# Kernel tuning notes

Measured on AMD Instinct MI355X. Metric: run time of the kernel, lower is better.

Reference implementation:

```python
import jax, jax.numpy as jnp
import numpy as np

B, N, D, F = 32, 4096, 256, 256

def setup_inputs() -> dict:
    key = jax.random.key(0)
    k1, k2, k3, k4 = jax.random.split(key, 4)
    raw_input = jax.random.normal(k1, (B, N, D), dtype=jnp.float32)
    input_plus_attention = jax.random.normal(k2, (B, F), dtype=jnp.float32)
    W = jax.random.normal(k3, (F, N), dtype=jnp.float32) * 0.02
    b = jnp.zeros((N,), dtype=jnp.float32)
    # keras 'uniform' initializer: U(-0.05, 0.05)
    threshold = jax.random.uniform(k4, (1,), minval=-0.05, maxval=0.05, dtype=jnp.float32)
    return {"raw_input": raw_input, "input_plus_attention": input_plus_attention,
            "W": W, "b": b, "threshold": threshold}

def reference(raw_input, input_plus_attention, W, b, threshold):
    # Dense(units, relu): [B,F] @ [F,N] -> [B,N]
    x = jax.nn.relu(input_plus_attention @ W + b)
    # BinaryLayer: 1.0 where x > threshold else 0.0 -> row selection mask [B,N]
    mask = x > threshold[0]
    # TF boolean_mask + reshape(B,-1,D) performs per-batch stream compaction of
    # selected rows. JAX needs static shapes, so compact selected rows to the
    # front (stable order preserved) and zero-pad the tail to length N.
    order = jnp.argsort(jnp.where(mask, 0, 1).astype(jnp.int32), axis=1)  # stable: selected first
    gathered = jnp.take_along_axis(raw_input, order[:, :, None], axis=1)  # [B,N,D]
    counts = jnp.sum(mask, axis=1, keepdims=True)                          # [B,1]
    keep = jnp.arange(N)[None, :] < counts                                 # [B,N]
    out = jnp.where(keep[:, :, None], gathered, jnp.zeros((), raw_input.dtype))
    return out
```

## Files before the change

### kernel.cpp

```cpp
#include <hip/hip_runtime.h>
#include <hip/hip_bf16.h>
#include <stdint.h>


#define BB 32
#define NN 4096
#define DD 256
#define FF 256
#define COLS 16
#define CH (NN / COLS)
#define ASTRIDE (FF + 4)
#define ROWS_PER_BLK 8

typedef float f4 __attribute__((ext_vector_type(4)));

__global__ __launch_bounds__(256) void mask_kernel(
    const float* __restrict__ A,
    const float* __restrict__ W,
    const float* __restrict__ bias,
    const float* __restrict__ thr_p,
    uint16_t* __restrict__ bits)
{
    __shared__ float a_sh[BB * ASTRIDE];
    __shared__ float wT[COLS * ASTRIDE];

    const int t     = threadIdx.x;
    const int chunk = blockIdx.x;
    const int n0    = chunk * COLS;

    for (int i = t; i < BB * FF; i += 256) {
        int b = i >> 8, f = i & 255;
        a_sh[b * ASTRIDE + f] = A[i];
    }
    for (int i = t; i < FF * COLS; i += 256) {
        int f = i >> 4, c = i & 15;
        wT[c * ASTRIDE + f] = W[(size_t)f * NN + n0 + c];
    }
    __syncthreads();

    const float thr = thr_p[0];
    const int c  = t & 15;
    const int b1 = t >> 4;
    const int b2 = b1 + 16;

    const f4* a1p = reinterpret_cast<const f4*>(a_sh + b1 * ASTRIDE);
    const f4* a2p = reinterpret_cast<const f4*>(a_sh + b2 * ASTRIDE);
    const f4* wp  = reinterpret_cast<const f4*>(wT   + c  * ASTRIDE);

    double s0 = 0.0, s1 = 0.0, s2 = 0.0, s3 = 0.0;
    #pragma unroll 8
    for (int fs = 0; fs < FF / 4; ++fs) {
        f4 w4 = wp[fs];
        f4 a1 = a1p[fs];
        f4 a2 = a2p[fs];
        s0 = fma((double)a1.x, (double)w4.x, s0);
        s0 = fma((double)a1.y, (double)w4.y, s0);
        s1 = fma((double)a1.z, (double)w4.z, s1);
        s1 = fma((double)a1.w, (double)w4.w, s1);
        s2 = fma((double)a2.x, (double)w4.x, s2);
        s2 = fma((double)a2.y, (double)w4.y, s2);
        s3 = fma((double)a2.z, (double)w4.z, s3);
        s3 = fma((double)a2.w, (double)w4.w, s3);
    }
    const float bi = bias[n0 + c];
    const float v1 = (float)(s0 + s1) + bi;
    const float v2 = (float)(s2 + s3) + bi;
    const int m1 = (fmaxf(v1, 0.f) > thr) ? 1 : 0;
    const int m2 = (fmaxf(v2, 0.f) > thr) ? 1 : 0;

    unsigned long long bal1 = __ballot(m1);
    unsigned long long bal2 = __ballot(m2);
    if (c == 0) {
        const int g = (t & 63) >> 4;
        bits[b1 * CH + chunk] = (uint16_t)((bal1 >> (16 * g)) & 0xFFFF);
        bits[b2 * CH + chunk] = (uint16_t)((bal2 >> (16 * g)) & 0xFFFF);
    }
}

__global__ __launch_bounds__(256) void gather_kernel(
    const float* __restrict__ raw,
    const uint16_t* __restrict__ bits,
    float* __restrict__ out)
{
    const int b   = blockIdx.y;
    const int t   = threadIdx.x;
    const int j0b = blockIdx.x * ROWS_PER_BLK;

    __shared__ int wsum[4];
    __shared__ int cnt_sh;
    __shared__ int order_sh[ROWS_PER_BLK];

    unsigned m = bits[b * CH + t];
    const int s = __popc(m);

    const int lane = t & 63;
    const int wid  = t >> 6;
    int incl = s;
    #pragma unroll
    for (int d = 1; d < 64; d <<= 1) {
        int x = __shfl_up(incl, d, 64);
        if (lane >= d) incl += x;
    }
    if (lane == 63) wsum[wid] = incl;
    __syncthreads();
    if (t == 0) {
        int run = 0;
        #pragma unroll
        for (int i = 0; i < 4; ++i) { int x = wsum[i]; wsum[i] = run; run += x; }
        cnt_sh = run;
    }
    __syncthreads();

    int base = wsum[wid] + (incl - s);
    if (base < j0b + ROWS_PER_BLK && base + s > j0b) {
        const int n0 = t * COLS;
        while (m) {
            const int pos = __ffs(m) - 1;
            const unsigned rel = (unsigned)(base - j0b);
            if (rel < ROWS_PER_BLK) order_sh[rel] = n0 + pos;
            ++base;
            if (base >= j0b + ROWS_PER_BLK) break;
            m &= m - 1;
        }
    }
    __syncthreads();

    const int cnt = cnt_sh;
    const f4* rawp = reinterpret_cast<const f4*>(raw);
    f4* outp = reinterpret_cast<f4*>(out);
    const int j0 = j0b + wid * 2;

    f4 r0 = {0.f, 0.f, 0.f, 0.f};
    f4 r1 = {0.f, 0.f, 0.f, 0.f};
    if (j0 < cnt) {
        const int src = order_sh[j0 - j0b];
        r0 = __builtin_nontemporal_load(rawp + ((size_t)b * NN + src) * (DD / 4) + lane);
    }
    if (j0 + 1 < cnt) {
        const int src = order_sh[j0 + 1 - j0b];
        r1 = __builtin_nontemporal_load(rawp + ((size_t)b * NN + src) * (DD / 4) + lane);
    }
    __builtin_nontemporal_store(r0, outp + ((size_t)b * NN + j0)     * (DD / 4) + lane);
    __builtin_nontemporal_store(r1, outp + ((size_t)b * NN + j0 + 1) * (DD / 4) + lane);
}

extern "C" void kernel_launch(void* const* d_in, const int* in_sizes, int n_in,
                              void* d_out, int out_size, void* d_ws, size_t ws_size,
                              hipStream_t stream) {
    const float* raw  = (const float*)d_in[0];
    const float* A    = (const float*)d_in[1];
    const float* W    = (const float*)d_in[2];
    const float* bias = (const float*)d_in[3];
    const float* thr  = (const float*)d_in[4];
    float* out = (float*)d_out;

    uint16_t* bits = (uint16_t*)d_ws;

    mask_kernel<<<CH, 256, 0, stream>>>(A, W, bias, thr, bits);
    gather_kernel<<<dim3(NN / ROWS_PER_BLK, BB), 256, 0, stream>>>(raw, bits, out);
}
```

Baseline: 61.45 us.

## Rebalance mask kernel to 8 columns and gather 32 rows per block

The mask kernel now handles 8 columns per block across 512 blocks, one batch row per thread, and writes byte-sized mask chunks that the gather kernel reads as 16-bit words. The gather kernel handles 32 output rows per block, eight per wave, and issues four independent loads before each group of stores. Loads switch from nontemporal to ordinary cached loads. The intent is more blocks for the GEMV mask stage, more memory-level parallelism in the gather, and less repeated prefix-scan work per block. The cost is fewer gather blocks and more registers per thread.

```diff
diff --git a/kernel.cpp b/kernel.cpp
--- a/kernel.cpp
+++ b/kernel.cpp
@@ -7,10 +7,8 @@
 #define NN 4096
 #define DD 256
 #define FF 256
-#define COLS 16
-#define CH (NN / COLS)
 #define ASTRIDE (FF + 4)
-#define ROWS_PER_BLK 8
+#define RPB 32
 
 typedef float f4 __attribute__((ext_vector_type(4)));
 
@@ -19,61 +17,49 @@
     const float* __restrict__ W,
     const float* __restrict__ bias,
     const float* __restrict__ thr_p,
-    uint16_t* __restrict__ bits)
+    uint8_t* __restrict__ bits8)
 {
     __shared__ float a_sh[BB * ASTRIDE];
-    __shared__ float wT[COLS * ASTRIDE];
+    __shared__ float wT[8 * ASTRIDE];
 
     const int t     = threadIdx.x;
     const int chunk = blockIdx.x;
-    const int n0    = chunk * COLS;
+    const int n0    = chunk * 8;
 
     for (int i = t; i < BB * FF; i += 256) {
         int b = i >> 8, f = i & 255;
         a_sh[b * ASTRIDE + f] = A[i];
     }
-    for (int i = t; i < FF * COLS; i += 256) {
-        int f = i >> 4, c = i & 15;
+    for (int i = t; i < FF * 8; i += 256) {
+        int f = i >> 3, c = i & 7;
         wT[c * ASTRIDE + f] = W[(size_t)f * NN + n0 + c];
     }
     __syncthreads();
 
     const float thr = thr_p[0];
-    const int c  = t & 15;
-    const int b1 = t >> 4;
-    const int b2 = b1 + 16;
+    const int c = t & 7;
+    const int b = t >> 3;
 
-    const f4* a1p = reinterpret_cast<const f4*>(a_sh + b1 * ASTRIDE);
-    const f4* a2p = reinterpret_cast<const f4*>(a_sh + b2 * ASTRIDE);
-    const f4* wp  = reinterpret_cast<const f4*>(wT   + c  * ASTRIDE);
+    const f4* ap = reinterpret_cast<const f4*>(a_sh + b * ASTRIDE);
+    const f4* wp = reinterpret_cast<const f4*>(wT   + c * ASTRIDE);
 
     double s0 = 0.0, s1 = 0.0, s2 = 0.0, s3 = 0.0;
     #pragma unroll 8
     for (int fs = 0; fs < FF / 4; ++fs) {
+        f4 a4 = ap[fs];
         f4 w4 = wp[fs];
-        f4 a1 = a1p[fs];
-        f4 a2 = a2p[fs];
-        s0 = fma((double)a1.x, (double)w4.x, s0);
-        s0 = fma((double)a1.y, (double)w4.y, s0);
-        s1 = fma((double)a1.z, (double)w4.z, s1);
-        s1 = fma((double)a1.w, (double)w4.w, s1);
-        s2 = fma((double)a2.x, (double)w4.x, s2);
-        s2 = fma((double)a2.y, (double)w4.y, s2);
-        s3 = fma((double)a2.z, (double)w4.z, s3);
-        s3 = fma((double)a2.w, (double)w4.w, s3);
+        s0 = fma((double)a4.x, (double)w4.x, s0);
+        s1 = fma((double)a4.y, (double)w4.y, s1);
+        s2 = fma((double)a4.z, (double)w4.z, s2);
+        s3 = fma((double)a4.w, (double)w4.w, s3);
     }
-    const float bi = bias[n0 + c];
-    const float v1 = (float)(s0 + s1) + bi;
-    const float v2 = (float)(s2 + s3) + bi;
-    const int m1 = (fmaxf(v1, 0.f) > thr) ? 1 : 0;
-    const int m2 = (fmaxf(v2, 0.f) > thr) ? 1 : 0;
+    const float v = (float)((s0 + s1) + (s2 + s3)) + bias[n0 + c];
+    const int m = (fmaxf(v, 0.f) > thr) ? 1 : 0;
 
-    unsigned long long bal1 = __ballot(m1);
-    unsigned long long bal2 = __ballot(m2);
+    unsigned long long bal = __ballot(m);
     if (c == 0) {
-        const int g = (t & 63) >> 4;
-        bits[b1 * CH + chunk] = (uint16_t)((bal1 >> (16 * g)) & 0xFFFF);
-        bits[b2 * CH + chunk] = (uint16_t)((bal2 >> (16 * g)) & 0xFFFF);
+        const int g = (t & 63) >> 3;
+        bits8[b * 512 + chunk] = (uint8_t)((bal >> (8 * g)) & 0xFF);
     }
 }
 
@@ -84,13 +70,13 @@
 {
     const int b   = blockIdx.y;
     const int t   = threadIdx.x;
-    const int j0b = blockIdx.x * ROWS_PER_BLK;
+    const int j0b = blockIdx.x * RPB;
 
     __shared__ int wsum[4];
     __shared__ int cnt_sh;
-    __shared__ int order_sh[ROWS_PER_BLK];
+    __shared__ int order_sh[RPB];
 
-    unsigned m = bits[b * CH + t];
+    unsigned m = bits[b * 256 + t];
     const int s = __popc(m);
 
     const int lane = t & 63;
@@ -112,36 +98,41 @@
     __syncthreads();
 
     int base = wsum[wid] + (incl - s);
-    if (base < j0b + ROWS_PER_BLK && base + s > j0b) {
-        const int n0 = t * COLS;
+    if (base < j0b + RPB && base + s > j0b) {
+        const int n0 = t * 16;
         while (m) {
             const int pos = __ffs(m) - 1;
             const unsigned rel = (unsigned)(base - j0b);
-            if (rel < ROWS_PER_BLK) order_sh[rel] = n0 + pos;
+            if (rel < RPB) order_sh[rel] = n0 + pos;
             ++base;
-            if (base >= j0b + ROWS_PER_BLK) break;
+            if (base >= j0b + RPB) break;
             m &= m - 1;
         }
     }
     __syncthreads();
 
     const int cnt = cnt_sh;
-    const f4* rawp = reinterpret_cast<const f4*>(raw);
-    f4* outp = reinterpret_cast<f4*>(out);
-    const int j0 = j0b + wid * 2;
+    const f4* rawb = reinterpret_cast<const f4*>(raw) + (size_t)b * NN * (DD / 4);
+    f4*       outb = reinterpret_cast<f4*>(out)       + (size_t)b * NN * (DD / 4);
+    const int j0 = j0b + wid * 8;
 
-    f4 r0 = {0.f, 0.f, 0.f, 0.f};
-    f4 r1 = {0.f, 0.f, 0.f, 0.f};
-    if (j0 < cnt) {
-        const int src = order_sh[j0 - j0b];
-        r0 = __builtin_nontemporal_load(rawp + ((size_t)b * NN + src) * (DD / 4) + lane);
+    #pragma unroll
+    for (int g = 0; g < 2; ++g) {
+        const int r = j0 + g * 4;
+        const int rr = r - j0b;
+        f4 v0 = {0.f, 0.f, 0.f, 0.f};
+        f4 v1 = {0.f, 0.f, 0.f, 0.f};
+        f4 v2 = {0.f, 0.f, 0.f, 0.f};
+        f4 v3 = {0.f, 0.f, 0.f, 0.f};
+        if (r + 0 < cnt) v0 = rawb[(size_t)order_sh[rr + 0] * (DD / 4) + lane];
+        if (r + 1 < cnt) v1 = rawb[(size_t)order_sh[rr + 1] * (DD / 4) + lane];
+        if (r + 2 < cnt) v2 = rawb[(size_t)order_sh[rr + 2] * (DD / 4) + lane];
+        if (r + 3 < cnt) v3 = rawb[(size_t)order_sh[rr + 3] * (DD / 4) + lane];
+        __builtin_nontemporal_store(v0, &outb[(size_t)(r + 0) * (DD / 4) + lane]);
+        __builtin_nontemporal_store(v1, &outb[(size_t)(r + 1) * (DD / 4) + lane]);
+        __builtin_nontemporal_store(v2, &outb[(size_t)(r + 2) * (DD / 4) + lane]);
+        __builtin_nontemporal_store(v3, &outb[(size_t)(r + 3) * (DD / 4) + lane]);
     }
-    if (j0 + 1 < cnt) {
-        const int src = order_sh[j0 + 1 - j0b];
-        r1 = __builtin_nontemporal_load(rawp + ((size_t)b * NN + src) * (DD / 4) + lane);
-    }
-    __builtin_nontemporal_store(r0, outp + ((size_t)b * NN + j0)     * (DD / 4) + lane);
-    __builtin_nontemporal_store(r1, outp + ((size_t)b * NN + j0 + 1) * (DD / 4) + lane);
 }
 
 extern "C" void kernel_launch(void* const* d_in, const int* in_sizes, int n_in,
@@ -154,8 +145,9 @@
     const float* thr  = (const float*)d_in[4];
     float* out = (float*)d_out;
 
-    uint16_t* bits = (uint16_t*)d_ws;
+    uint8_t* bits8 = (uint8_t*)d_ws;
 
-    mask_kernel<<<CH, 256, 0, stream>>>(A, W, bias, thr, bits);
-    gather_kernel<<<dim3(NN / ROWS_PER_BLK, BB), 256, 0, stream>>>(raw, bits, out);
+    mask_kernel<<<512, 256, 0, stream>>>(A, W, bias, thr, bits8);
+    gather_kernel<<<dim3(NN / RPB, BB), 256, 0, stream>>>(
+        raw, (const uint16_t*)bits8, out);
 }
```

New measurement: 55.85 us. -9.1%, faster.
